# Performance work log

Measured on AMD Instinct MI355X. Metric: run time of the kernel, lower is better.

Reference implementation:

```python
import jax, jax.numpy as jnp
import numpy as np

N_NODES = 100000
N_EDGES = 1600000
D_IN, D_HID, D_OUT = 128, 64, 16


def _glorot(key, shape):
    lim = float(np.sqrt(6.0 / (shape[0] + shape[1])))
    return jax.random.uniform(key, shape, jnp.float32, -lim, lim)


def setup_inputs() -> dict:
    key = jax.random.key(0)
    k1, k2, k3 = jax.random.split(key, 3)
    x = jax.random.normal(k1, (N_NODES, D_IN), dtype=jnp.float32)
    edge_index = jax.random.randint(k2, (2, N_EDGES), 0, N_NODES, dtype=jnp.int64)
    kw1, kw2 = jax.random.split(k3)
    W1 = _glorot(kw1, (D_IN, D_HID))
    b1 = jnp.zeros((D_HID,), jnp.float32)
    W2 = _glorot(kw2, (D_HID, D_OUT))
    b2 = jnp.zeros((D_OUT,), jnp.float32)
    return {"x": x, "edge_index": edge_index, "W1": W1, "b1": b1, "W2": W2, "b2": b2}


def _gcn_conv(h, W, b, src, dst, norm, n_nodes):
    # PyG GCNConv: linear first, then normalized neighbor aggregation, then bias.
    h = h @ W                                        # [N, d_out]
    msg = h[src] * norm[:, None]                     # gather over edges(+self loops)
    out = jax.ops.segment_sum(msg, dst, num_segments=n_nodes)  # scatter-add
    return out + b


def reference(x, edge_index, W1, b1, W2, b2):
    n = x.shape[0]
    loop = jnp.arange(n, dtype=edge_index.dtype)
    src = jnp.concatenate([edge_index[0], loop])     # add self loops
    dst = jnp.concatenate([edge_index[1], loop])
    # symmetric normalization D^-1/2 (A+I) D^-1/2
    deg = jax.ops.segment_sum(jnp.ones(src.shape[0], x.dtype), dst, num_segments=n)
    dinv = jnp.where(deg > 0, jax.lax.rsqrt(jnp.maximum(deg, 1e-12)), 0.0)
    norm = dinv[src] * dinv[dst]                     # [E+N]

    out = _gcn_conv(x, W1, b1, src, dst, norm, n)
    out = jax.nn.sigmoid(out)
    # dropout p=0.5 with training=False -> identity (eval mode)
    out = _gcn_conv(out, W2, b2, src, dst, norm, n)
    return jax.nn.log_softmax(out, axis=1)
```

## Files before the change

kernel.cpp:

```cpp
#include <hip/hip_runtime.h>
#include <hip/hip_bf16.h>


constexpr int D_IN  = 128;
constexpr int D_HID = 64;
constexpr int D_OUT = 16;

constexpr int WSHIFT  = 9;
constexpr int MAXB    = 256;
constexpr int BCAP    = 12288;
constexpr int CSRCAP  = 16384;
constexpr int BIN_CAP = 48;
constexpr int CHUNK   = 4096;

typedef __attribute__((ext_vector_type(8))) short bf16x8;
typedef __attribute__((ext_vector_type(4))) float f32x4;

__device__ inline float bflo(unsigned u){ return __uint_as_float(u << 16); }
__device__ inline float bfhi(unsigned u){ return __uint_as_float(u & 0xffff0000u); }
__device__ inline unsigned f2bu(float f){
    __hip_bfloat16 h = __float2bfloat16(f);
    return (unsigned)*reinterpret_cast<unsigned short*>(&h);
}
__device__ inline float sigf(float x){ return 1.0f / (1.0f + __expf(-x)); }

__global__ __launch_bounds__(256) void k_bucketize(
    const int* __restrict__ ei, const unsigned* __restrict__ xraw,
    int* __restrict__ flags, unsigned* __restrict__ gcur,
    unsigned* __restrict__ gbuf, int ne, int B)
{
    __shared__ unsigned bcnt[MAXB];
    __shared__ unsigned bbase[MAXB];
    __shared__ unsigned bins[MAXB * BIN_CAP];
    __shared__ int s_i64;

    const int t = threadIdx.x, lane = t & 63, wv = t >> 6;
    const int e0 = blockIdx.x * CHUNK;

    if (t < MAXB) bcnt[t] = 0u;
    if (wv == 0){
        int w = ei[2 * lane + 1];
        unsigned long long m = __ballot(w == 0);
        if (lane == 0) s_i64 = (__popcll(m) > 48) ? 1 : 0;
        if (blockIdx.x == 0){
            unsigned u = xraw[lane];
            unsigned h0 = u & 0xffffu, h1 = u >> 16;
            unsigned ex0 = (h0 >> 7) & 0xffu, ex1 = (h1 >> 7) & 0xffu;
            bool bad0 = !((h0 & 0x7fffu) == 0 || (ex0 >= 97 && ex0 <= 157));
            bool bad1 = !((h1 & 0x7fffu) == 0 || (ex1 >= 97 && ex1 <= 157));
            unsigned long long m0 = __ballot(bad0);
            unsigned long long m1 = __ballot(bad1);
            if (lane == 0){
                int bad = __popcll(m0) + __popcll(m1);
                flags[0] = (bad > 8) ? 0 : 1;
                flags[1] = s_i64;
            }
        }
    }
    __syncthreads();
    const int i64 = s_i64;
    const bool vec = ((ne & 1) == 0);

    #pragma unroll
    for (int k = 0; k < CHUNK / 512; ++k){
        int e = e0 + k * 512 + 2 * t;
        int s0, d0, s1, d1;
        int cntE = 0;
        if (vec && e < ne){
            if (i64){
                int4 sp = *(const int4*)&ei[2 * e];
                int4 dp = *(const int4*)&ei[2 * (ne + e)];
                s0 = sp.x; s1 = sp.z; d0 = dp.x; d1 = dp.z;
            } else {
                int2 sp = *(const int2*)&ei[e];
                int2 dp = *(const int2*)&ei[ne + e];
                s0 = sp.x; s1 = sp.y; d0 = dp.x; d1 = dp.y;
            }
            cntE = 2;
        } else {
            if (e < ne){
                if (i64){ s0 = ei[2*e]; d0 = ei[2*(ne+e)]; }
                else    { s0 = ei[e];   d0 = ei[ne+e]; }
                cntE = 1;
                if (e + 1 < ne){
                    if (i64){ s1 = ei[2*(e+1)]; d1 = ei[2*(ne+e+1)]; }
                    else    { s1 = ei[e+1];     d1 = ei[ne+e+1]; }
                    cntE = 2;
                }
            }
        }
        #pragma unroll
        for (int j = 0; j < 2; ++j){
            if (j < cntE){
                int s = j ? s1 : s0, d = j ? d1 : d0;
                int b = d >> WSHIFT;
                unsigned v = ((unsigned)s << WSHIFT) | ((unsigned)d & ((1u << WSHIFT) - 1));
                unsigned p = atomicAdd(&bcnt[b], 1u);
                if (p < (unsigned)BIN_CAP){
                    bins[b * BIN_CAP + p] = v;
                } else {
                    unsigned g = atomicAdd(&gcur[b], 1u);
                    gbuf[(size_t)b * BCAP + g] = v;
                }
            }
        }
    }
    __syncthreads();

    if (t < B){
        unsigned c = min(bcnt[t], (unsigned)BIN_CAP);
        bbase[t] = atomicAdd(&gcur[t], c);
    }
    __syncthreads();

    for (int b = wv; b < B; b += 4){
        unsigned c = min(bcnt[b], (unsigned)BIN_CAP);
        for (unsigned o = lane; o < c; o += 64)
            gbuf[(size_t)b * BCAP + bbase[b] + o] = bins[b * BIN_CAP + o];
    }
}

__global__ __launch_bounds__(1024) void k_build(
    const unsigned* __restrict__ gbuf, const unsigned* __restrict__ gcnt,
    unsigned* __restrict__ off, unsigned* __restrict__ offend,
    float* __restrict__ dinv, int* __restrict__ csr, int n, int B)
{
    __shared__ unsigned hist[512];
    __shared__ unsigned offl[512];
    __shared__ unsigned wsums[8];

    const int t = threadIdx.x, lane = t & 63, wv = t >> 6;
    const int b = blockIdx.x;
    const int base = b << WSHIFT;
    const int nodes = min(512, n - base);
    const unsigned bb = (unsigned)b * CSRCAP;

    if (t < 512) hist[t] = 0u;
    __syncthreads();
    const unsigned cnt = gcnt[b];
    const unsigned* mybuf = gbuf + (size_t)b * BCAP;

    for (unsigned i = t; i < cnt; i += 1024)
        atomicAdd(&hist[mybuf[i] & ((1u << WSHIFT) - 1)], 1u);
    __syncthreads();

    unsigned v = 0, p = 0, x = 0;
    if (t < 512){
        v = hist[t];
        p = (v + 7u) & ~7u;
        x = p;
        #pragma unroll
        for (int o = 1; o < 64; o <<= 1){
            unsigned y = __shfl_up(x, o, 64);
            if (lane >= o) x += y;
        }
        if (lane == 63) wsums[wv] = x;
    }
    __syncthreads();
    if (t == 0){
        unsigned run = 0;
        #pragma unroll
        for (int w = 0; w < 8; ++w){ unsigned tv = wsums[w]; wsums[w] = run; run += tv; }
    }
    __syncthreads();
    if (t < 512) offl[t] = x - p + wsums[wv];
    __syncthreads();

    if (t < nodes){
        off[base + t]    = bb + offl[t];
        offend[base + t] = bb + offl[t] + p;
        dinv[base + t]   = rsqrtf(1.0f + (float)v);
    }
    __syncthreads();

    if (t < 512) hist[t] = offl[t];
    __syncthreads();

    for (unsigned i = t; i < cnt; i += 1024){
        unsigned rec = mybuf[i];
        unsigned pos = atomicAdd(&hist[rec & ((1u << WSHIFT) - 1)], 1u);
        csr[bb + pos] = (int)(rec >> WSHIFT);
    }
    __syncthreads();

    if (t < nodes){
        unsigned s = offl[t] + v, e2 = offl[t] + p;
        for (unsigned j = s; j < e2; ++j) csr[bb + j] = n;
    }
}

__global__ __launch_bounds__(256) void k_linear1(
    const unsigned* __restrict__ xraw, const unsigned* __restrict__ w1raw,
    const int* __restrict__ flags, const float* __restrict__ dinv,
    unsigned short* __restrict__ h1s, int n)
{
    const int lane = threadIdx.x & 63;
    const int wv   = threadIdx.x >> 6;
    const int m = lane & 15, q = lane >> 4;
    const int isBf16 = flags[0];

    if (blockIdx.x == 0 && threadIdx.x < 16)
        ((uint2*)(h1s + (size_t)n * D_HID))[threadIdx.x] = make_uint2(0u, 0u);

    bf16x8 bfr[4][4];
    if (isBf16){
        const unsigned short* w = (const unsigned short*)w1raw;
        #pragma unroll
        for (int kc = 0; kc < 4; ++kc)
            #pragma unroll
            for (int ct = 0; ct < 4; ++ct)
                #pragma unroll
                for (int j = 0; j < 8; ++j)
                    bfr[kc][ct][j] = (short)w[(kc*32 + q*8 + j) * D_HID + ct*16 + m];
    } else {
        const float* w = (const float*)w1raw;
        #pragma unroll
        for (int kc = 0; kc < 4; ++kc)
            #pragma unroll
            for (int ct = 0; ct < 4; ++ct)
                #pragma unroll
                for (int j = 0; j < 8; ++j)
                    bfr[kc][ct][j] = (short)f2bu(w[(kc*32 + q*8 + j) * D_HID + ct*16 + m]);
    }

    const int ntiles = (n + 15) >> 4;
    for (int tile = blockIdx.x * 4 + wv; tile < ntiles; tile += gridDim.x * 4){
        const int node0 = tile << 4;
        int arow = node0 + m; if (arow >= n) arow = n - 1;
        f32x4 ac0 = {0,0,0,0}, ac1 = {0,0,0,0}, ac2 = {0,0,0,0}, ac3 = {0,0,0,0};
        #pragma unroll
        for (int kc = 0; kc < 4; ++kc){
            bf16x8 a;
            if (isBf16){
                uint4 u = *(const uint4*)((const unsigned short*)xraw + (size_t)arow * D_IN + kc*32 + q*8);
                a = *reinterpret_cast<bf16x8*>(&u);
            } else {
                const float* xp = (const float*)xraw + (size_t)arow * D_IN + kc*32 + q*8;
                float4 f0 = *(const float4*)xp;
                float4 f1 = *(const float4*)(xp + 4);
                a[0]=(short)f2bu(f0.x); a[1]=(short)f2bu(f0.y); a[2]=(short)f2bu(f0.z); a[3]=(short)f2bu(f0.w);
                a[4]=(short)f2bu(f1.x); a[5]=(short)f2bu(f1.y); a[6]=(short)f2bu(f1.z); a[7]=(short)f2bu(f1.w);
            }
            ac0 = __builtin_amdgcn_mfma_f32_16x16x32_bf16(a, bfr[kc][0], ac0, 0, 0, 0);
            ac1 = __builtin_amdgcn_mfma_f32_16x16x32_bf16(a, bfr[kc][1], ac1, 0, 0, 0);
            ac2 = __builtin_amdgcn_mfma_f32_16x16x32_bf16(a, bfr[kc][2], ac2, 0, 0, 0);
            ac3 = __builtin_amdgcn_mfma_f32_16x16x32_bf16(a, bfr[kc][3], ac3, 0, 0, 0);
        }
        #pragma unroll
        for (int i = 0; i < 4; ++i){
            int nr = node0 + q*4 + i;
            if (nr < n){
                float di = dinv[nr];
                unsigned short* o = h1s + (size_t)nr * D_HID + m;
                o[0]  = (unsigned short)f2bu(ac0[i] * di);
                o[16] = (unsigned short)f2bu(ac1[i] * di);
                o[32] = (unsigned short)f2bu(ac2[i] * di);
                o[48] = (unsigned short)f2bu(ac3[i] * di);
            }
        }
    }
}

__global__ __launch_bounds__(256) void k_aggA(
    const unsigned* __restrict__ off, const unsigned* __restrict__ offend,
    const int* __restrict__ csr_src,
    const float* __restrict__ dinv, const unsigned short* __restrict__ h1s,
    const unsigned* __restrict__ b1raw, const unsigned* __restrict__ w2raw,
    const int* __restrict__ flags,
    unsigned short* __restrict__ h2s, int n)
{
    __shared__ unsigned short act_s[16][72];

    const int lane = threadIdx.x & 63;
    const int wv   = threadIdx.x >> 6;
    const int grp  = lane >> 4;
    const int f    = lane & 15;
    const int dl   = wv * 4 + grp;
    const int d    = blockIdx.x * 16 + dl;
    const int isBf16 = flags[0];

    bf16x8 w2f[2];
    if (wv == 0){
        const int m0 = lane & 15, q0 = lane >> 4;
        if (isBf16){
            const unsigned short* w = (const unsigned short*)w2raw;
            #pragma unroll
            for (int kc = 0; kc < 2; ++kc)
                #pragma unroll
                for (int j = 0; j < 8; ++j)
                    w2f[kc][j] = (short)w[(kc*32 + q0*8 + j) * D_OUT + m0];
        } else {
            const float* w = (const float*)w2raw;
            #pragma unroll
            for (int kc = 0; kc < 2; ++kc)
                #pragma unroll
                for (int j = 0; j < 8; ++j)
                    w2f[kc][j] = (short)f2bu(w[(kc*32 + q0*8 + j) * D_OUT + m0]);
        }
        if (blockIdx.x == 0 && lane < 4)
            ((uint2*)(h2s + (size_t)n * D_OUT))[lane] = make_uint2(0u, 0u);
    }

    if (d < n){
        const int beg = (int)off[d], end = (int)offend[d];
        float a0=0.f, a1=0.f, a2=0.f, a3=0.f;
        for (int i = beg; i < end; i += 8){
            uint4 cA = *(const uint4*)&csr_src[i];
            uint4 cB = *(const uint4*)&csr_src[i + 4];
            uint2 u0 = *(const uint2*)&h1s[(size_t)(unsigned)cA.x * D_HID + f * 4];
            uint2 u1 = *(const uint2*)&h1s[(size_t)(unsigned)cA.y * D_HID + f * 4];
            uint2 u2 = *(const uint2*)&h1s[(size_t)(unsigned)cA.z * D_HID + f * 4];
            uint2 u3 = *(const uint2*)&h1s[(size_t)(unsigned)cA.w * D_HID + f * 4];
            uint2 u4 = *(const uint2*)&h1s[(size_t)(unsigned)cB.x * D_HID + f * 4];
            uint2 u5 = *(const uint2*)&h1s[(size_t)(unsigned)cB.y * D_HID + f * 4];
            uint2 u6 = *(const uint2*)&h1s[(size_t)(unsigned)cB.z * D_HID + f * 4];
            uint2 u7 = *(const uint2*)&h1s[(size_t)(unsigned)cB.w * D_HID + f * 4];
            a0 += bflo(u0.x) + bflo(u1.x) + bflo(u2.x) + bflo(u3.x)
                + bflo(u4.x) + bflo(u5.x) + bflo(u6.x) + bflo(u7.x);
            a1 += bfhi(u0.x) + bfhi(u1.x) + bfhi(u2.x) + bfhi(u3.x)
                + bfhi(u4.x) + bfhi(u5.x) + bfhi(u6.x) + bfhi(u7.x);
            a2 += bflo(u0.y) + bflo(u1.y) + bflo(u2.y) + bflo(u3.y)
                + bflo(u4.y) + bflo(u5.y) + bflo(u6.y) + bflo(u7.y);
            a3 += bfhi(u0.y) + bfhi(u1.y) + bfhi(u2.y) + bfhi(u3.y)
                + bfhi(u4.y) + bfhi(u5.y) + bfhi(u6.y) + bfhi(u7.y);
        }
        uint2 su = *(const uint2*)&h1s[(size_t)d * D_HID + f * 4];
        a0 += bflo(su.x); a1 += bfhi(su.x);
        a2 += bflo(su.y); a3 += bfhi(su.y);
        const float dd = dinv[d];
        float b0, b1v, b2v, b3v;
        if (isBf16){
            uint2 bu = ((const uint2*)b1raw)[f];
            b0 = bflo(bu.x); b1v = bfhi(bu.x); b2v = bflo(bu.y); b3v = bfhi(bu.y);
        } else {
            float4 bb = ((const float4*)b1raw)[f];
            b0 = bb.x; b1v = bb.y; b2v = bb.z; b3v = bb.w;
        }
        act_s[dl][f*4+0] = (unsigned short)f2bu(sigf(fmaf(a0, dd, b0)));
        act_s[dl][f*4+1] = (unsigned short)f2bu(sigf(fmaf(a1, dd, b1v)));
        act_s[dl][f*4+2] = (unsigned short)f2bu(sigf(fmaf(a2, dd, b2v)));
        act_s[dl][f*4+3] = (unsigned short)f2bu(sigf(fmaf(a3, dd, b3v)));
    } else {
        #pragma unroll
        for (int j = 0; j < 4; ++j) act_s[dl][f*4+j] = 0;
    }
    __syncthreads();

    if (wv == 0){
        const int m0 = lane & 15, q0 = lane >> 4;
        f32x4 acc = {0,0,0,0};
        #pragma unroll
        for (int kc = 0; kc < 2; ++kc){
            bf16x8 a;
            #pragma unroll
            for (int j = 0; j < 8; ++j)
                a[j] = (short)act_s[m0][kc*32 + q0*8 + j];
            acc = __builtin_amdgcn_mfma_f32_16x16x32_bf16(a, w2f[kc], acc, 0, 0, 0);
        }
        #pragma unroll
        for (int i = 0; i < 4; ++i){
            int nr = blockIdx.x * 16 + q0*4 + i;
            if (nr < n)
                h2s[(size_t)nr * D_OUT + m0] = (unsigned short)f2bu(acc[i] * dinv[nr]);
        }
    }
}

__global__ __launch_bounds__(256) void k_aggB(
    const unsigned* __restrict__ off, const unsigned* __restrict__ offend,
    const int* __restrict__ csr_src,
    const float* __restrict__ dinv, const unsigned short* __restrict__ h2s,
    const unsigned* __restrict__ b2raw, const int* __restrict__ flags,
    void* __restrict__ out, int n)
{
    const int lane = threadIdx.x & 63;
    const int wv   = threadIdx.x >> 6;
    const int grp  = lane >> 2;
    const int f    = lane & 3;
    const int d    = (blockIdx.x * 4 + wv) * 16 + grp;
    const int isBf16 = flags[0];
    if (d >= n) return;

    const int beg = (int)off[d], end = (int)offend[d];
    float a0=0.f, a1=0.f, a2=0.f, a3=0.f;
    for (int i = beg; i < end; i += 8){
        uint4 cA = *(const uint4*)&csr_src[i];
        uint4 cB = *(const uint4*)&csr_src[i + 4];
        uint2 u0 = *(const uint2*)&h2s[(size_t)(unsigned)cA.x * D_OUT + f * 4];
        uint2 u1 = *(const uint2*)&h2s[(size_t)(unsigned)cA.y * D_OUT + f * 4];
        uint2 u2 = *(const uint2*)&h2s[(size_t)(unsigned)cA.z * D_OUT + f * 4];
        uint2 u3 = *(const uint2*)&h2s[(size_t)(unsigned)cA.w * D_OUT + f * 4];
        uint2 u4 = *(const uint2*)&h2s[(size_t)(unsigned)cB.x * D_OUT + f * 4];
        uint2 u5 = *(const uint2*)&h2s[(size_t)(unsigned)cB.y * D_OUT + f * 4];
        uint2 u6 = *(const uint2*)&h2s[(size_t)(unsigned)cB.z * D_OUT + f * 4];
        uint2 u7 = *(const uint2*)&h2s[(size_t)(unsigned)cB.w * D_OUT + f * 4];
        a0 += bflo(u0.x) + bflo(u1.x) + bflo(u2.x) + bflo(u3.x)
            + bflo(u4.x) + bflo(u5.x) + bflo(u6.x) + bflo(u7.x);
        a1 += bfhi(u0.x) + bfhi(u1.x) + bfhi(u2.x) + bfhi(u3.x)
            + bfhi(u4.x) + bfhi(u5.x) + bfhi(u6.x) + bfhi(u7.x);
        a2 += bflo(u0.y) + bflo(u1.y) + bflo(u2.y) + bflo(u3.y)
            + bflo(u4.y) + bflo(u5.y) + bflo(u6.y) + bflo(u7.y);
        a3 += bfhi(u0.y) + bfhi(u1.y) + bfhi(u2.y) + bfhi(u3.y)
            + bfhi(u4.y) + bfhi(u5.y) + bfhi(u6.y) + bfhi(u7.y);
    }
    uint2 su = *(const uint2*)&h2s[(size_t)d * D_OUT + f * 4];
    a0 += bflo(su.x); a1 += bfhi(su.x);
    a2 += bflo(su.y); a3 += bfhi(su.y);
    const float dd = dinv[d];
    float b0, b1v, b2v, b3v;
    if (isBf16){
        uint2 bu = ((const uint2*)b2raw)[f];
        b0 = bflo(bu.x); b1v = bfhi(bu.x); b2v = bflo(bu.y); b3v = bfhi(bu.y);
    } else {
        float4 bb = ((const float4*)b2raw)[f];
        b0 = bb.x; b1v = bb.y; b2v = bb.z; b3v = bb.w;
    }
    a0 = fmaf(a0, dd, b0); a1 = fmaf(a1, dd, b1v);
    a2 = fmaf(a2, dd, b2v); a3 = fmaf(a3, dd, b3v);
    float m = fmaxf(fmaxf(a0, a1), fmaxf(a2, a3));
    m = fmaxf(m, __shfl_xor(m, 1, 4));
    m = fmaxf(m, __shfl_xor(m, 2, 4));
    float s = __expf(a0 - m) + __expf(a1 - m) + __expf(a2 - m) + __expf(a3 - m);
    s += __shfl_xor(s, 1, 4);
    s += __shfl_xor(s, 2, 4);
    float ls = m + __logf(s);
    if (isBf16){
        uint2 pk;
        pk.x = f2bu(a0 - ls) | (f2bu(a1 - ls) << 16);
        pk.y = f2bu(a2 - ls) | (f2bu(a3 - ls) << 16);
        *(uint2*)((__hip_bfloat16*)out + (size_t)d * D_OUT + f * 4) = pk;
    } else {
        float4 o4 = make_float4(a0 - ls, a1 - ls, a2 - ls, a3 - ls);
        *(float4*)((float*)out + (size_t)d * D_OUT + f * 4) = o4;
    }
}

extern "C" void kernel_launch(void* const* d_in, const int* in_sizes, int n_in,
                              void* d_out, int out_size, void* d_ws, size_t ws_size,
                              hipStream_t stream)
{
    const unsigned* xraw  = (const unsigned*)d_in[0];
    const int*      ei    = (const int*)d_in[1];
    const unsigned* w1raw = (const unsigned*)d_in[2];
    const unsigned* b1raw = (const unsigned*)d_in[3];
    const unsigned* w2raw = (const unsigned*)d_in[4];
    const unsigned* b2raw = (const unsigned*)d_in[5];

    const int n  = in_sizes[0] / D_IN;
    const int ne = in_sizes[1] / 2;
    const int B  = (n + ((1 << WSHIFT) - 1)) >> WSHIFT;

    size_t nAl = ((size_t)n + 255) & ~(size_t)255;
    int*            flags  = (int*)d_ws;
    unsigned*       gcur   = (unsigned*)d_ws + 64;
    float*          dinv   = (float*)(gcur + 256);
    unsigned*       off    = (unsigned*)(dinv + nAl);
    unsigned*       offend = off + nAl;
    int*            csr    = (int*)(offend + nAl);
    unsigned*       gbuf   = (unsigned*)(csr + (size_t)MAXB * CSRCAP);
    unsigned short* h1s    = (unsigned short*)(gbuf + (size_t)MAXB * BCAP);
    unsigned short* h2s    = h1s + (size_t)(n + 16) * D_HID;

    const int nchunk  = (ne + CHUNK - 1) / CHUNK;
    const int ntiles1 = (n + 15) / 16;
    const int grid1   = (ntiles1 + 3) / 4;

    hipMemsetAsync(gcur, 0, MAXB * sizeof(unsigned), stream);
    k_bucketize <<<nchunk, 256, 0, stream>>>(ei, xraw, flags, gcur, gbuf, ne, B);
    k_build     <<<B, 1024, 0, stream>>>(gbuf, gcur, off, offend, dinv, csr, n, B);

    k_linear1   <<<grid1, 256, 0, stream>>>(xraw, w1raw, flags, dinv, h1s, n);
    k_aggA      <<<(n + 15) / 16, 256, 0, stream>>>(off, offend, csr, dinv, h1s, b1raw, w2raw, flags, h2s, n);
    k_aggB      <<<(n + 63) / 64, 256, 0, stream>>>(off, offend, csr, dinv, h2s, b2raw, flags, d_out, n);
}
```

Baseline: 194.6 us.

## Fuse all GCN stages into one persistent kernel with grid-wide barriers

Replaces the five separate launches (bucketize, CSR build, linear1, layer-1 aggregation, layer-2 aggregation) with one persistent kernel sized at three blocks per CU. Atomic-counter grid barriers separate the phases, and each phase loops over its work items with a grid stride. This removes launch gaps and tail effects between stages. In exchange, the CSR build now runs on 256-thread blocks instead of 1024, the shared bins and chunk sizes are halved to fit the higher occupancy, and correctness relies on all blocks being co-resident for the spin barriers.

```diff
diff --git a/kernel.cpp b/kernel.cpp
--- a/kernel.cpp
+++ b/kernel.cpp
@@ -10,8 +10,8 @@
 constexpr int MAXB    = 256;
 constexpr int BCAP    = 12288;
 constexpr int CSRCAP  = 16384;
-constexpr int BIN_CAP = 48;
-constexpr int CHUNK   = 4096;
+constexpr int BIN_CAP = 24;
+constexpr int CHUNK   = 2048;
 
 typedef __attribute__((ext_vector_type(8))) short bf16x8;
 typedef __attribute__((ext_vector_type(4))) float f32x4;
@@ -24,20 +24,35 @@
 }
 __device__ inline float sigf(float x){ return 1.0f / (1.0f + __expf(-x)); }
 
-__global__ __launch_bounds__(256) void k_bucketize(
-    const int* __restrict__ ei, const unsigned* __restrict__ xraw,
-    int* __restrict__ flags, unsigned* __restrict__ gcur,
-    unsigned* __restrict__ gbuf, int ne, int B)
+__device__ inline void gbar(unsigned* ctr){
+    __syncthreads();
+    if (threadIdx.x == 0){
+        __threadfence();
+        __hip_atomic_fetch_add(ctr, 1u, __ATOMIC_RELEASE, __HIP_MEMORY_SCOPE_AGENT);
+        while (__hip_atomic_load(ctr, __ATOMIC_RELAXED, __HIP_MEMORY_SCOPE_AGENT) < gridDim.x)
+            __builtin_amdgcn_s_sleep(16);
+        __threadfence();
+    }
+    __syncthreads();
+}
+
+__global__ __launch_bounds__(256, 4) void k_mega(
+    const unsigned* __restrict__ xraw, const int* __restrict__ ei,
+    const unsigned* __restrict__ w1raw, const unsigned* __restrict__ b1raw,
+    const unsigned* __restrict__ w2raw, const unsigned* __restrict__ b2raw,
+    int* __restrict__ flags, unsigned* __restrict__ bar,
+    unsigned* __restrict__ gcur, unsigned* __restrict__ gbuf,
+    unsigned* __restrict__ off, unsigned* __restrict__ offend,
+    float* __restrict__ dinv, int* __restrict__ csr,
+    unsigned short* __restrict__ h1s, unsigned short* __restrict__ h2s,
+    void* __restrict__ out, int n, int ne, int B, int nchunk)
 {
-    __shared__ unsigned bcnt[MAXB];
-    __shared__ unsigned bbase[MAXB];
-    __shared__ unsigned bins[MAXB * BIN_CAP];
+    __shared__ unsigned smem[512 + MAXB * BIN_CAP];
     __shared__ int s_i64;
 
     const int t = threadIdx.x, lane = t & 63, wv = t >> 6;
-    const int e0 = blockIdx.x * CHUNK;
-
-    if (t < MAXB) bcnt[t] = 0u;
+    const int G = (int)gridDim.x;
+
     if (wv == 0){
         int w = ei[2 * lane + 1];
         unsigned long long m = __ballot(w == 0);
@@ -61,377 +76,362 @@
     const int i64 = s_i64;
     const bool vec = ((ne & 1) == 0);
 
-    #pragma unroll
-    for (int k = 0; k < CHUNK / 512; ++k){
-        int e = e0 + k * 512 + 2 * t;
-        int s0, d0, s1, d1;
-        int cntE = 0;
-        if (vec && e < ne){
-            if (i64){
-                int4 sp = *(const int4*)&ei[2 * e];
-                int4 dp = *(const int4*)&ei[2 * (ne + e)];
-                s0 = sp.x; s1 = sp.z; d0 = dp.x; d1 = dp.z;
+    {
+        unsigned* bcnt  = smem;
+        unsigned* bbase = smem + 256;
+        unsigned* bins  = smem + 512;
+
+        for (int ch = (int)blockIdx.x; ch < nchunk; ch += G){
+            if (t < MAXB) bcnt[t] = 0u;
+            __syncthreads();
+            const int e0 = ch * CHUNK;
+            #pragma unroll
+            for (int k = 0; k < CHUNK / 512; ++k){
+                int e = e0 + k * 512 + 2 * t;
+                int s0, d0, s1, d1;
+                int cntE = 0;
+                if (vec && e < ne){
+                    if (i64){
+                        int4 sp = *(const int4*)&ei[2 * e];
+                        int4 dp = *(const int4*)&ei[2 * (ne + e)];
+                        s0 = sp.x; s1 = sp.z; d0 = dp.x; d1 = dp.z;
+                    } else {
+                        int2 sp = *(const int2*)&ei[e];
+                        int2 dp = *(const int2*)&ei[ne + e];
+                        s0 = sp.x; s1 = sp.y; d0 = dp.x; d1 = dp.y;
+                    }
+                    cntE = 2;
+                } else {
+                    if (e < ne){
+                        if (i64){ s0 = ei[2*e]; d0 = ei[2*(ne+e)]; }
+                        else    { s0 = ei[e];   d0 = ei[ne+e]; }
+                        cntE = 1;
+                        if (e + 1 < ne){
+                            if (i64){ s1 = ei[2*(e+1)]; d1 = ei[2*(ne+e+1)]; }
+                            else    { s1 = ei[e+1];     d1 = ei[ne+e+1]; }
+                            cntE = 2;
+                        }
+                    }
+                }
+                #pragma unroll
+                for (int j = 0; j < 2; ++j){
+                    if (j < cntE){
+                        int s = j ? s1 : s0, d = j ? d1 : d0;
+                        int b = d >> WSHIFT;
+                        unsigned v = ((unsigned)s << WSHIFT) | ((unsigned)d & ((1u << WSHIFT) - 1));
+                        unsigned p = atomicAdd(&bcnt[b], 1u);
+                        if (p < (unsigned)BIN_CAP){
+                            bins[b * BIN_CAP + p] = v;
+                        } else {
+                            unsigned g2 = atomicAdd(&gcur[b], 1u);
+                            gbuf[(size_t)b * BCAP + g2] = v;
+                        }
+                    }
+                }
+            }
+            __syncthreads();
+            if (t < B){
+                unsigned c = min(bcnt[t], (unsigned)BIN_CAP);
+                bbase[t] = atomicAdd(&gcur[t], c);
+            }
+            __syncthreads();
+            for (int b = wv; b < B; b += 4){
+                unsigned c = min(bcnt[b], (unsigned)BIN_CAP);
+                unsigned ba = bbase[b];
+                for (unsigned o = (unsigned)lane; o < c; o += 64)
+                    gbuf[(size_t)b * BCAP + ba + o] = bins[b * BIN_CAP + o];
+            }
+            __syncthreads();
+        }
+    }
+
+    gbar(&bar[0]);
+
+    {
+        unsigned* hist  = smem;
+        unsigned* wsums = smem + 512;
+        for (int b = (int)blockIdx.x; b < B; b += G){
+            const int base = b << WSHIFT;
+            const int nodes = min(512, n - base);
+            const unsigned bb = (unsigned)b * CSRCAP;
+            hist[t] = 0u; hist[t + 256] = 0u;
+            __syncthreads();
+            const unsigned cnt = gcur[b];
+            const unsigned* mybuf = gbuf + (size_t)b * BCAP;
+            for (unsigned i = t; i < cnt; i += 256)
+                atomicAdd(&hist[mybuf[i] & ((1u << WSHIFT) - 1)], 1u);
+            __syncthreads();
+            unsigned v0 = hist[2*t], v1 = hist[2*t+1];
+            unsigned p0 = (v0 + 7u) & ~7u, p1 = (v1 + 7u) & ~7u;
+            unsigned x = p0 + p1, xi = x;
+            #pragma unroll
+            for (int o = 1; o < 64; o <<= 1){
+                unsigned y = __shfl_up(xi, o, 64);
+                if (lane >= o) xi += y;
+            }
+            if (lane == 63) wsums[wv] = xi;
+            __syncthreads();
+            if (t == 0){
+                unsigned run = 0;
+                #pragma unroll
+                for (int w8 = 0; w8 < 4; ++w8){ unsigned tv = wsums[w8]; wsums[w8] = run; run += tv; }
+            }
+            __syncthreads();
+            const unsigned ex = xi - x + wsums[wv];
+            if (2*t < nodes){
+                off[base + 2*t]    = bb + ex;
+                offend[base + 2*t] = bb + ex + p0;
+                dinv[base + 2*t]   = rsqrtf(1.0f + (float)v0);
+            }
+            if (2*t+1 < nodes){
+                off[base + 2*t+1]    = bb + ex + p0;
+                offend[base + 2*t+1] = bb + ex + p0 + p1;
+                dinv[base + 2*t+1]   = rsqrtf(1.0f + (float)v1);
+            }
+            __syncthreads();
+            hist[2*t] = ex; hist[2*t+1] = ex + p0;
+            __syncthreads();
+            for (unsigned i = t; i < cnt; i += 256){
+                unsigned rec = mybuf[i];
+                unsigned pos = atomicAdd(&hist[rec & ((1u << WSHIFT) - 1)], 1u);
+                csr[bb + pos] = (int)(rec >> WSHIFT);
+            }
+            __syncthreads();
+            if (2*t < nodes){
+                for (unsigned j2 = ex + v0; j2 < ex + p0; ++j2) csr[bb + j2] = n;
+            }
+            if (2*t+1 < nodes){
+                unsigned o1 = ex + p0;
+                for (unsigned j2 = o1 + v1; j2 < o1 + p1; ++j2) csr[bb + j2] = n;
+            }
+            __syncthreads();
+        }
+    }
+
+    gbar(&bar[1]);
+
+    const int isBf16 = flags[0];
+    if (blockIdx.x == 0 && t < 16)
+        ((uint2*)(h1s + (size_t)n * D_HID))[t] = make_uint2(0u, 0u);
+    {
+        const int m = lane & 15, q = lane >> 4;
+        const int ntiles = (n + 15) >> 4;
+        for (int tile = (int)blockIdx.x * 4 + wv; tile < ntiles; tile += G * 4){
+            const int node0 = tile << 4;
+            int arow = node0 + m; if (arow >= n) arow = n - 1;
+            f32x4 ac0 = {0,0,0,0}, ac1 = {0,0,0,0}, ac2 = {0,0,0,0}, ac3 = {0,0,0,0};
+            #pragma unroll
+            for (int kc = 0; kc < 4; ++kc){
+                bf16x8 a;
+                if (isBf16){
+                    uint4 u = *(const uint4*)((const unsigned short*)xraw + (size_t)arow * D_IN + kc*32 + q*8);
+                    a = *reinterpret_cast<bf16x8*>(&u);
+                } else {
+                    const float* xp = (const float*)xraw + (size_t)arow * D_IN + kc*32 + q*8;
+                    float4 f0 = *(const float4*)xp;
+                    float4 f1 = *(const float4*)(xp + 4);
+                    a[0]=(short)f2bu(f0.x); a[1]=(short)f2bu(f0.y); a[2]=(short)f2bu(f0.z); a[3]=(short)f2bu(f0.w);
+                    a[4]=(short)f2bu(f1.x); a[5]=(short)f2bu(f1.y); a[6]=(short)f2bu(f1.z); a[7]=(short)f2bu(f1.w);
+                }
+                bf16x8 b0, b1, b2, b3;
+                if (isBf16){
+                    const unsigned short* w = (const unsigned short*)w1raw;
+                    #pragma unroll
+                    for (int j = 0; j < 8; ++j){
+                        int r = (kc*32 + q*8 + j) * D_HID + m;
+                        b0[j] = (short)w[r];      b1[j] = (short)w[r + 16];
+                        b2[j] = (short)w[r + 32]; b3[j] = (short)w[r + 48];
+                    }
+                } else {
+                    const float* w = (const float*)w1raw;
+                    #pragma unroll
+                    for (int j = 0; j < 8; ++j){
+                        int r = (kc*32 + q*8 + j) * D_HID + m;
+                        b0[j] = (short)f2bu(w[r]);      b1[j] = (short)f2bu(w[r + 16]);
+                        b2[j] = (short)f2bu(w[r + 32]); b3[j] = (short)f2bu(w[r + 48]);
+                    }
+                }
+                ac0 = __builtin_amdgcn_mfma_f32_16x16x32_bf16(a, b0, ac0, 0, 0, 0);
+                ac1 = __builtin_amdgcn_mfma_f32_16x16x32_bf16(a, b1, ac1, 0, 0, 0);
+                ac2 = __builtin_amdgcn_mfma_f32_16x16x32_bf16(a, b2, ac2, 0, 0, 0);
+                ac3 = __builtin_amdgcn_mfma_f32_16x16x32_bf16(a, b3, ac3, 0, 0, 0);
+            }
+            #pragma unroll
+            for (int i = 0; i < 4; ++i){
+                int nr = node0 + q*4 + i;
+                if (nr < n){
+                    float di = dinv[nr];
+                    unsigned short* o = h1s + (size_t)nr * D_HID + m;
+                    o[0]  = (unsigned short)f2bu(ac0[i] * di);
+                    o[16] = (unsigned short)f2bu(ac1[i] * di);
+                    o[32] = (unsigned short)f2bu(ac2[i] * di);
+                    o[48] = (unsigned short)f2bu(ac3[i] * di);
+                }
+            }
+        }
+    }
+
+    gbar(&bar[2]);
+
+    {
+        unsigned short* act_s = (unsigned short*)smem;
+        const int grp = lane >> 4;
+        const int f   = lane & 15;
+        const int dl  = wv * 4 + grp;
+        const int m0 = lane & 15, q0 = lane >> 4;
+
+        bf16x8 w2f[2];
+        if (wv == 0){
+            if (isBf16){
+                const unsigned short* w = (const unsigned short*)w2raw;
+                #pragma unroll
+                for (int kc = 0; kc < 2; ++kc)
+                    #pragma unroll
+                    for (int j = 0; j < 8; ++j)
+                        w2f[kc][j] = (short)w[(kc*32 + q0*8 + j) * D_OUT + m0];
             } else {
-                int2 sp = *(const int2*)&ei[e];
-                int2 dp = *(const int2*)&ei[ne + e];
-                s0 = sp.x; s1 = sp.y; d0 = dp.x; d1 = dp.y;
-            }
-            cntE = 2;
-        } else {
-            if (e < ne){
-                if (i64){ s0 = ei[2*e]; d0 = ei[2*(ne+e)]; }
-                else    { s0 = ei[e];   d0 = ei[ne+e]; }
-                cntE = 1;
-                if (e + 1 < ne){
-                    if (i64){ s1 = ei[2*(e+1)]; d1 = ei[2*(ne+e+1)]; }
-                    else    { s1 = ei[e+1];     d1 = ei[ne+e+1]; }
-                    cntE = 2;
-                }
-            }
-        }
-        #pragma unroll
-        for (int j = 0; j < 2; ++j){
-            if (j < cntE){
-                int s = j ? s1 : s0, d = j ? d1 : d0;
-                int b = d >> WSHIFT;
-                unsigned v = ((unsigned)s << WSHIFT) | ((unsigned)d & ((1u << WSHIFT) - 1));
-                unsigned p = atomicAdd(&bcnt[b], 1u);
-                if (p < (unsigned)BIN_CAP){
-                    bins[b * BIN_CAP + p] = v;
+                const float* w = (const float*)w2raw;
+                #pragma unroll
+                for (int kc = 0; kc < 2; ++kc)
+                    #pragma unroll
+                    for (int j = 0; j < 8; ++j)
+                        w2f[kc][j] = (short)f2bu(w[(kc*32 + q0*8 + j) * D_OUT + m0]);
+            }
+            if (blockIdx.x == 0 && lane < 4)
+                ((uint2*)(h2s + (size_t)n * D_OUT))[lane] = make_uint2(0u, 0u);
+        }
+
+        const int ng = (n + 15) >> 4;
+        for (int g = (int)blockIdx.x; g < ng; g += G){
+            const int d = g * 16 + dl;
+            if (d < n){
+                const int beg = (int)off[d], end = (int)offend[d];
+                float a0=0.f, a1=0.f, a2=0.f, a3=0.f;
+                for (int i = beg; i < end; i += 8){
+                    uint4 cA = *(const uint4*)&csr[i];
+                    uint4 cB = *(const uint4*)&csr[i + 4];
+                    uint2 u0 = *(const uint2*)&h1s[(size_t)(unsigned)cA.x * D_HID + f * 4];
+                    uint2 u1 = *(const uint2*)&h1s[(size_t)(unsigned)cA.y * D_HID + f * 4];
+                    uint2 u2 = *(const uint2*)&h1s[(size_t)(unsigned)cA.z * D_HID + f * 4];
+                    uint2 u3 = *(const uint2*)&h1s[(size_t)(unsigned)cA.w * D_HID + f * 4];
+                    uint2 u4 = *(const uint2*)&h1s[(size_t)(unsigned)cB.x * D_HID + f * 4];
+                    uint2 u5 = *(const uint2*)&h1s[(size_t)(unsigned)cB.y * D_HID + f * 4];
+                    uint2 u6 = *(const uint2*)&h1s[(size_t)(unsigned)cB.z * D_HID + f * 4];
+                    uint2 u7 = *(const uint2*)&h1s[(size_t)(unsigned)cB.w * D_HID + f * 4];
+                    a0 += bflo(u0.x) + bflo(u1.x) + bflo(u2.x) + bflo(u3.x)
+                        + bflo(u4.x) + bflo(u5.x) + bflo(u6.x) + bflo(u7.x);
+                    a1 += bfhi(u0.x) + bfhi(u1.x) + bfhi(u2.x) + bfhi(u3.x)
+                        + bfhi(u4.x) + bfhi(u5.x) + bfhi(u6.x) + bfhi(u7.x);
+                    a2 += bflo(u0.y) + bflo(u1.y) + bflo(u2.y) + bflo(u3.y)
+                        + bflo(u4.y) + bflo(u5.y) + bflo(u6.y) + bflo(u7.y);
+                    a3 += bfhi(u0.y) + bfhi(u1.y) + bfhi(u2.y) + bfhi(u3.y)
+                        + bfhi(u4.y) + bfhi(u5.y) + bfhi(u6.y) + bfhi(u7.y);
+                }
+                uint2 su = *(const uint2*)&h1s[(size_t)d * D_HID + f * 4];
+                a0 += bflo(su.x); a1 += bfhi(su.x);
+                a2 += bflo(su.y); a3 += bfhi(su.y);
+                const float dd = dinv[d];
+                float b0, b1v, b2v, b3v;
+                if (isBf16){
+                    uint2 bu = ((const uint2*)b1raw)[f];
+                    b0 = bflo(bu.x); b1v = bfhi(bu.x); b2v = bflo(bu.y); b3v = bfhi(bu.y);
                 } else {
-                    unsigned g = atomicAdd(&gcur[b], 1u);
-                    gbuf[(size_t)b * BCAP + g] = v;
-                }
-            }
-        }
-    }
-    __syncthreads();
-
-    if (t < B){
-        unsigned c = min(bcnt[t], (unsigned)BIN_CAP);
-        bbase[t] = atomicAdd(&gcur[t], c);
-    }
-    __syncthreads();
-
-    for (int b = wv; b < B; b += 4){
-        unsigned c = min(bcnt[b], (unsigned)BIN_CAP);
-        for (unsigned o = lane; o < c; o += 64)
-            gbuf[(size_t)b * BCAP + bbase[b] + o] = bins[b * BIN_CAP + o];
-    }
-}
-
-__global__ __launch_bounds__(1024) void k_build(
-    const unsigned* __restrict__ gbuf, const unsigned* __restrict__ gcnt,
-    unsigned* __restrict__ off, unsigned* __restrict__ offend,
-    float* __restrict__ dinv, int* __restrict__ csr, int n, int B)
-{
-    __shared__ unsigned hist[512];
-    __shared__ unsigned offl[512];
-    __shared__ unsigned wsums[8];
-
-    const int t = threadIdx.x, lane = t & 63, wv = t >> 6;
-    const int b = blockIdx.x;
-    const int base = b << WSHIFT;
-    const int nodes = min(512, n - base);
-    const unsigned bb = (unsigned)b * CSRCAP;
-
-    if (t < 512) hist[t] = 0u;
-    __syncthreads();
-    const unsigned cnt = gcnt[b];
-    const unsigned* mybuf = gbuf + (size_t)b * BCAP;
-
-    for (unsigned i = t; i < cnt; i += 1024)
-        atomicAdd(&hist[mybuf[i] & ((1u << WSHIFT) - 1)], 1u);
-    __syncthreads();
-
-    unsigned v = 0, p = 0, x = 0;
-    if (t < 512){
-        v = hist[t];
-        p = (v + 7u) & ~7u;
-        x = p;
-        #pragma unroll
-        for (int o = 1; o < 64; o <<= 1){
-            unsigned y = __shfl_up(x, o, 64);
-            if (lane >= o) x += y;
-        }
-        if (lane == 63) wsums[wv] = x;
-    }
-    __syncthreads();
-    if (t == 0){
-        unsigned run = 0;
-        #pragma unroll
-        for (int w = 0; w < 8; ++w){ unsigned tv = wsums[w]; wsums[w] = run; run += tv; }
-    }
-    __syncthreads();
-    if (t < 512) offl[t] = x - p + wsums[wv];
-    __syncthreads();
-
-    if (t < nodes){
-        off[base + t]    = bb + offl[t];
-        offend[base + t] = bb + offl[t] + p;
-        dinv[base + t]   = rsqrtf(1.0f + (float)v);
-    }
-    __syncthreads();
-
-    if (t < 512) hist[t] = offl[t];
-    __syncthreads();
-
-    for (unsigned i = t; i < cnt; i += 1024){
-        unsigned rec = mybuf[i];
-        unsigned pos = atomicAdd(&hist[rec & ((1u << WSHIFT) - 1)], 1u);
-        csr[bb + pos] = (int)(rec >> WSHIFT);
-    }
-    __syncthreads();
-
-    if (t < nodes){
-        unsigned s = offl[t] + v, e2 = offl[t] + p;
-        for (unsigned j = s; j < e2; ++j) csr[bb + j] = n;
-    }
-}
-
-__global__ __launch_bounds__(256) void k_linear1(
-    const unsigned* __restrict__ xraw, const unsigned* __restrict__ w1raw,
-    const int* __restrict__ flags, const float* __restrict__ dinv,
-    unsigned short* __restrict__ h1s, int n)
-{
-    const int lane = threadIdx.x & 63;
-    const int wv   = threadIdx.x >> 6;
-    const int m = lane & 15, q = lane >> 4;
-    const int isBf16 = flags[0];
-
-    if (blockIdx.x == 0 && threadIdx.x < 16)
-        ((uint2*)(h1s + (size_t)n * D_HID))[threadIdx.x] = make_uint2(0u, 0u);
-
-    bf16x8 bfr[4][4];
-    if (isBf16){
-        const unsigned short* w = (const unsigned short*)w1raw;
-        #pragma unroll
-        for (int kc = 0; kc < 4; ++kc)
-            #pragma unroll
-            for (int ct = 0; ct < 4; ++ct)
-                #pragma unroll
-                for (int j = 0; j < 8; ++j)
-                    bfr[kc][ct][j] = (short)w[(kc*32 + q*8 + j) * D_HID + ct*16 + m];
-    } else {
-        const float* w = (const float*)w1raw;
-        #pragma unroll
-        for (int kc = 0; kc < 4; ++kc)
-            #pragma unroll
-            for (int ct = 0; ct < 4; ++ct)
-                #pragma unroll
-                for (int j = 0; j < 8; ++j)
-                    bfr[kc][ct][j] = (short)f2bu(w[(kc*32 + q*8 + j) * D_HID + ct*16 + m]);
-    }
-
-    const int ntiles = (n + 15) >> 4;
-    for (int tile = blockIdx.x * 4 + wv; tile < ntiles; tile += gridDim.x * 4){
-        const int node0 = tile << 4;
-        int arow = node0 + m; if (arow >= n) arow = n - 1;
-        f32x4 ac0 = {0,0,0,0}, ac1 = {0,0,0,0}, ac2 = {0,0,0,0}, ac3 = {0,0,0,0};
-        #pragma unroll
-        for (int kc = 0; kc < 4; ++kc){
-            bf16x8 a;
+                    float4 bb4 = ((const float4*)b1raw)[f];
+                    b0 = bb4.x; b1v = bb4.y; b2v = bb4.z; b3v = bb4.w;
+                }
+                act_s[dl*72 + f*4 + 0] = (unsigned short)f2bu(sigf(fmaf(a0, dd, b0)));
+                act_s[dl*72 + f*4 + 1] = (unsigned short)f2bu(sigf(fmaf(a1, dd, b1v)));
+                act_s[dl*72 + f*4 + 2] = (unsigned short)f2bu(sigf(fmaf(a2, dd, b2v)));
+                act_s[dl*72 + f*4 + 3] = (unsigned short)f2bu(sigf(fmaf(a3, dd, b3v)));
+            } else {
+                #pragma unroll
+                for (int j = 0; j < 4; ++j) act_s[dl*72 + f*4 + j] = 0;
+            }
+            __syncthreads();
+
+            if (wv == 0){
+                f32x4 acc = {0,0,0,0};
+                #pragma unroll
+                for (int kc = 0; kc < 2; ++kc){
+                    bf16x8 a;
+                    #pragma unroll
+                    for (int j = 0; j < 8; ++j)
+                        a[j] = (short)act_s[m0*72 + kc*32 + q0*8 + j];
+                    acc = __builtin_amdgcn_mfma_f32_16x16x32_bf16(a, w2f[kc], acc, 0, 0, 0);
+                }
+                #pragma unroll
+                for (int i = 0; i < 4; ++i){
+                    int nr = g * 16 + q0*4 + i;
+                    if (nr < n)
+                        h2s[(size_t)nr * D_OUT + m0] = (unsigned short)f2bu(acc[i] * dinv[nr]);
+                }
+            }
+            __syncthreads();
+        }
+    }
+
+    gbar(&bar[3]);
+
+    {
+        const int grp = lane >> 2;
+        const int f   = lane & 3;
+        const int nw = (n + 15) >> 4;
+        for (int w = (int)blockIdx.x * 4 + wv; w < nw; w += G * 4){
+            const int d = w * 16 + grp;
+            if (d >= n) continue;
+            const int beg = (int)off[d], end = (int)offend[d];
+            float a0=0.f, a1=0.f, a2=0.f, a3=0.f;
+            for (int i = beg; i < end; i += 8){
+                uint4 cA = *(const uint4*)&csr[i];
+                uint4 cB = *(const uint4*)&csr[i + 4];
+                uint2 u0 = *(const uint2*)&h2s[(size_t)(unsigned)cA.x * D_OUT + f * 4];
+                uint2 u1 = *(const uint2*)&h2s[(size_t)(unsigned)cA.y * D_OUT + f * 4];
+                uint2 u2 = *(const uint2*)&h2s[(size_t)(unsigned)cA.z * D_OUT + f * 4];
+                uint2 u3 = *(const uint2*)&h2s[(size_t)(unsigned)cA.w * D_OUT + f * 4];
+                uint2 u4 = *(const uint2*)&h2s[(size_t)(unsigned)cB.x * D_OUT + f * 4];
+                uint2 u5 = *(const uint2*)&h2s[(size_t)(unsigned)cB.y * D_OUT + f * 4];
+                uint2 u6 = *(const uint2*)&h2s[(size_t)(unsigned)cB.z * D_OUT + f * 4];
+                uint2 u7 = *(const uint2*)&h2s[(size_t)(unsigned)cB.w * D_OUT + f * 4];
+                a0 += bflo(u0.x) + bflo(u1.x) + bflo(u2.x) + bflo(u3.x)
+                    + bflo(u4.x) + bflo(u5.x) + bflo(u6.x) + bflo(u7.x);
+                a1 += bfhi(u0.x) + bfhi(u1.x) + bfhi(u2.x) + bfhi(u3.x)
+                    + bfhi(u4.x) + bfhi(u5.x) + bfhi(u6.x) + bfhi(u7.x);
+                a2 += bflo(u0.y) + bflo(u1.y) + bflo(u2.y) + bflo(u3.y)
+                    + bflo(u4.y) + bflo(u5.y) + bflo(u6.y) + bflo(u7.y);
+                a3 += bfhi(u0.y) + bfhi(u1.y) + bfhi(u2.y) + bfhi(u3.y)
+                    + bfhi(u4.y) + bfhi(u5.y) + bfhi(u6.y) + bfhi(u7.y);
+            }
+            uint2 su = *(const uint2*)&h2s[(size_t)d * D_OUT + f * 4];
+            a0 += bflo(su.x); a1 += bfhi(su.x);
+            a2 += bflo(su.y); a3 += bfhi(su.y);
+            const float dd = dinv[d];
+            float b0, b1v, b2v, b3v;
             if (isBf16){
-                uint4 u = *(const uint4*)((const unsigned short*)xraw + (size_t)arow * D_IN + kc*32 + q*8);
-                a = *reinterpret_cast<bf16x8*>(&u);
+                uint2 bu = ((const uint2*)b2raw)[f];
+                b0 = bflo(bu.x); b1v = bfhi(bu.x); b2v = bflo(bu.y); b3v = bfhi(bu.y);
             } else {
-                const float* xp = (const float*)xraw + (size_t)arow * D_IN + kc*32 + q*8;
-                float4 f0 = *(const float4*)xp;
-                float4 f1 = *(const float4*)(xp + 4);
-                a[0]=(short)f2bu(f0.x); a[1]=(short)f2bu(f0.y); a[2]=(short)f2bu(f0.z); a[3]=(short)f2bu(f0.w);
-                a[4]=(short)f2bu(f1.x); a[5]=(short)f2bu(f1.y); a[6]=(short)f2bu(f1.z); a[7]=(short)f2bu(f1.w);
-            }
-            ac0 = __builtin_amdgcn_mfma_f32_16x16x32_bf16(a, bfr[kc][0], ac0, 0, 0, 0);
-            ac1 = __builtin_amdgcn_mfma_f32_16x16x32_bf16(a, bfr[kc][1], ac1, 0, 0, 0);
-            ac2 = __builtin_amdgcn_mfma_f32_16x16x32_bf16(a, bfr[kc][2], ac2, 0, 0, 0);
-            ac3 = __builtin_amdgcn_mfma_f32_16x16x32_bf16(a, bfr[kc][3], ac3, 0, 0, 0);
-        }
-        #pragma unroll
-        for (int i = 0; i < 4; ++i){
-            int nr = node0 + q*4 + i;
-            if (nr < n){
-                float di = dinv[nr];
-                unsigned short* o = h1s + (size_t)nr * D_HID + m;
-                o[0]  = (unsigned short)f2bu(ac0[i] * di);
-                o[16] = (unsigned short)f2bu(ac1[i] * di);
-                o[32] = (unsigned short)f2bu(ac2[i] * di);
-                o[48] = (unsigned short)f2bu(ac3[i] * di);
-            }
-        }
-    }
-}
-
-__global__ __launch_bounds__(256) void k_aggA(
-    const unsigned* __restrict__ off, const unsigned* __restrict__ offend,
-    const int* __restrict__ csr_src,
-    const float* __restrict__ dinv, const unsigned short* __restrict__ h1s,
-    const unsigned* __restrict__ b1raw, const unsigned* __restrict__ w2raw,
-    const int* __restrict__ flags,
-    unsigned short* __restrict__ h2s, int n)
-{
-    __shared__ unsigned short act_s[16][72];
-
-    const int lane = threadIdx.x & 63;
-    const int wv   = threadIdx.x >> 6;
-    const int grp  = lane >> 4;
-    const int f    = lane & 15;
-    const int dl   = wv * 4 + grp;
-    const int d    = blockIdx.x * 16 + dl;
-    const int isBf16 = flags[0];
-
-    bf16x8 w2f[2];
-    if (wv == 0){
-        const int m0 = lane & 15, q0 = lane >> 4;
-        if (isBf16){
-            const unsigned short* w = (const unsigned short*)w2raw;
-            #pragma unroll
-            for (int kc = 0; kc < 2; ++kc)
-                #pragma unroll
-                for (int j = 0; j < 8; ++j)
-                    w2f[kc][j] = (short)w[(kc*32 + q0*8 + j) * D_OUT + m0];
-        } else {
-            const float* w = (const float*)w2raw;
-            #pragma unroll
-            for (int kc = 0; kc < 2; ++kc)
-                #pragma unroll
-                for (int j = 0; j < 8; ++j)
-                    w2f[kc][j] = (short)f2bu(w[(kc*32 + q0*8 + j) * D_OUT + m0]);
-        }
-        if (blockIdx.x == 0 && lane < 4)
-            ((uint2*)(h2s + (size_t)n * D_OUT))[lane] = make_uint2(0u, 0u);
-    }
-
-    if (d < n){
-        const int beg = (int)off[d], end = (int)offend[d];
-        float a0=0.f, a1=0.f, a2=0.f, a3=0.f;
-        for (int i = beg; i < end; i += 8){
-            uint4 cA = *(const uint4*)&csr_src[i];
-            uint4 cB = *(const uint4*)&csr_src[i + 4];
-            uint2 u0 = *(const uint2*)&h1s[(size_t)(unsigned)cA.x * D_HID + f * 4];
-            uint2 u1 = *(const uint2*)&h1s[(size_t)(unsigned)cA.y * D_HID + f * 4];
-            uint2 u2 = *(const uint2*)&h1s[(size_t)(unsigned)cA.z * D_HID + f * 4];
-            uint2 u3 = *(const uint2*)&h1s[(size_t)(unsigned)cA.w * D_HID + f * 4];
-            uint2 u4 = *(const uint2*)&h1s[(size_t)(unsigned)cB.x * D_HID + f * 4];
-            uint2 u5 = *(const uint2*)&h1s[(size_t)(unsigned)cB.y * D_HID + f * 4];
-            uint2 u6 = *(const uint2*)&h1s[(size_t)(unsigned)cB.z * D_HID + f * 4];
-            uint2 u7 = *(const uint2*)&h1s[(size_t)(unsigned)cB.w * D_HID + f * 4];
-            a0 += bflo(u0.x) + bflo(u1.x) + bflo(u2.x) + bflo(u3.x)
-                + bflo(u4.x) + bflo(u5.x) + bflo(u6.x) + bflo(u7.x);
-            a1 += bfhi(u0.x) + bfhi(u1.x) + bfhi(u2.x) + bfhi(u3.x)
-                + bfhi(u4.x) + bfhi(u5.x) + bfhi(u6.x) + bfhi(u7.x);
-            a2 += bflo(u0.y) + bflo(u1.y) + bflo(u2.y) + bflo(u3.y)
-                + bflo(u4.y) + bflo(u5.y) + bflo(u6.y) + bflo(u7.y);
-            a3 += bfhi(u0.y) + bfhi(u1.y) + bfhi(u2.y) + bfhi(u3.y)
-                + bfhi(u4.y) + bfhi(u5.y) + bfhi(u6.y) + bfhi(u7.y);
-        }
-        uint2 su = *(const uint2*)&h1s[(size_t)d * D_HID + f * 4];
-        a0 += bflo(su.x); a1 += bfhi(su.x);
-        a2 += bflo(su.y); a3 += bfhi(su.y);
-        const float dd = dinv[d];
-        float b0, b1v, b2v, b3v;
-        if (isBf16){
-            uint2 bu = ((const uint2*)b1raw)[f];
-            b0 = bflo(bu.x); b1v = bfhi(bu.x); b2v = bflo(bu.y); b3v = bfhi(bu.y);
-        } else {
-            float4 bb = ((const float4*)b1raw)[f];
-            b0 = bb.x; b1v = bb.y; b2v = bb.z; b3v = bb.w;
-        }
-        act_s[dl][f*4+0] = (unsigned short)f2bu(sigf(fmaf(a0, dd, b0)));
-        act_s[dl][f*4+1] = (unsigned short)f2bu(sigf(fmaf(a1, dd, b1v)));
-        act_s[dl][f*4+2] = (unsigned short)f2bu(sigf(fmaf(a2, dd, b2v)));
-        act_s[dl][f*4+3] = (unsigned short)f2bu(sigf(fmaf(a3, dd, b3v)));
-    } else {
-        #pragma unroll
-        for (int j = 0; j < 4; ++j) act_s[dl][f*4+j] = 0;
-    }
-    __syncthreads();
-
-    if (wv == 0){
-        const int m0 = lane & 15, q0 = lane >> 4;
-        f32x4 acc = {0,0,0,0};
-        #pragma unroll
-        for (int kc = 0; kc < 2; ++kc){
-            bf16x8 a;
-            #pragma unroll
-            for (int j = 0; j < 8; ++j)
-                a[j] = (short)act_s[m0][kc*32 + q0*8 + j];
-            acc = __builtin_amdgcn_mfma_f32_16x16x32_bf16(a, w2f[kc], acc, 0, 0, 0);
-        }
-        #pragma unroll
-        for (int i = 0; i < 4; ++i){
-            int nr = blockIdx.x * 16 + q0*4 + i;
-            if (nr < n)
-                h2s[(size_t)nr * D_OUT + m0] = (unsigned short)f2bu(acc[i] * dinv[nr]);
-        }
-    }
-}
-
-__global__ __launch_bounds__(256) void k_aggB(
-    const unsigned* __restrict__ off, const unsigned* __restrict__ offend,
-    const int* __restrict__ csr_src,
-    const float* __restrict__ dinv, const unsigned short* __restrict__ h2s,
-    const unsigned* __restrict__ b2raw, const int* __restrict__ flags,
-    void* __restrict__ out, int n)
-{
-    const int lane = threadIdx.x & 63;
-    const int wv   = threadIdx.x >> 6;
-    const int grp  = lane >> 2;
-    const int f    = lane & 3;
-    const int d    = (blockIdx.x * 4 + wv) * 16 + grp;
-    const int isBf16 = flags[0];
-    if (d >= n) return;
-
-    const int beg = (int)off[d], end = (int)offend[d];
-    float a0=0.f, a1=0.f, a2=0.f, a3=0.f;
-    for (int i = beg; i < end; i += 8){
-        uint4 cA = *(const uint4*)&csr_src[i];
-        uint4 cB = *(const uint4*)&csr_src[i + 4];
-        uint2 u0 = *(const uint2*)&h2s[(size_t)(unsigned)cA.x * D_OUT + f * 4];
-        uint2 u1 = *(const uint2*)&h2s[(size_t)(unsigned)cA.y * D_OUT + f * 4];
-        uint2 u2 = *(const uint2*)&h2s[(size_t)(unsigned)cA.z * D_OUT + f * 4];
-        uint2 u3 = *(const uint2*)&h2s[(size_t)(unsigned)cA.w * D_OUT + f * 4];
-        uint2 u4 = *(const uint2*)&h2s[(size_t)(unsigned)cB.x * D_OUT + f * 4];
-        uint2 u5 = *(const uint2*)&h2s[(size_t)(unsigned)cB.y * D_OUT + f * 4];
-        uint2 u6 = *(const uint2*)&h2s[(size_t)(unsigned)cB.z * D_OUT + f * 4];
-        uint2 u7 = *(const uint2*)&h2s[(size_t)(unsigned)cB.w * D_OUT + f * 4];
-        a0 += bflo(u0.x) + bflo(u1.x) + bflo(u2.x) + bflo(u3.x)
-            + bflo(u4.x) + bflo(u5.x) + bflo(u6.x) + bflo(u7.x);
-        a1 += bfhi(u0.x) + bfhi(u1.x) + bfhi(u2.x) + bfhi(u3.x)
-            + bfhi(u4.x) + bfhi(u5.x) + bfhi(u6.x) + bfhi(u7.x);
-        a2 += bflo(u0.y) + bflo(u1.y) + bflo(u2.y) + bflo(u3.y)
-            + bflo(u4.y) + bflo(u5.y) + bflo(u6.y) + bflo(u7.y);
-        a3 += bfhi(u0.y) + bfhi(u1.y) + bfhi(u2.y) + bfhi(u3.y)
-            + bfhi(u4.y) + bfhi(u5.y) + bfhi(u6.y) + bfhi(u7.y);
-    }
-    uint2 su = *(const uint2*)&h2s[(size_t)d * D_OUT + f * 4];
-    a0 += bflo(su.x); a1 += bfhi(su.x);
-    a2 += bflo(su.y); a3 += bfhi(su.y);
-    const float dd = dinv[d];
-    float b0, b1v, b2v, b3v;
-    if (isBf16){
-        uint2 bu = ((const uint2*)b2raw)[f];
-        b0 = bflo(bu.x); b1v = bfhi(bu.x); b2v = bflo(bu.y); b3v = bfhi(bu.y);
-    } else {
-        float4 bb = ((const float4*)b2raw)[f];
-        b0 = bb.x; b1v = bb.y; b2v = bb.z; b3v = bb.w;
-    }
-    a0 = fmaf(a0, dd, b0); a1 = fmaf(a1, dd, b1v);
-    a2 = fmaf(a2, dd, b2v); a3 = fmaf(a3, dd, b3v);
-    float m = fmaxf(fmaxf(a0, a1), fmaxf(a2, a3));
-    m = fmaxf(m, __shfl_xor(m, 1, 4));
-    m = fmaxf(m, __shfl_xor(m, 2, 4));
-    float s = __expf(a0 - m) + __expf(a1 - m) + __expf(a2 - m) + __expf(a3 - m);
-    s += __shfl_xor(s, 1, 4);
-    s += __shfl_xor(s, 2, 4);
-    float ls = m + __logf(s);
-    if (isBf16){
-        uint2 pk;
-        pk.x = f2bu(a0 - ls) | (f2bu(a1 - ls) << 16);
-        pk.y = f2bu(a2 - ls) | (f2bu(a3 - ls) << 16);
-        *(uint2*)((__hip_bfloat16*)out + (size_t)d * D_OUT + f * 4) = pk;
-    } else {
-        float4 o4 = make_float4(a0 - ls, a1 - ls, a2 - ls, a3 - ls);
-        *(float4*)((float*)out + (size_t)d * D_OUT + f * 4) = o4;
+                float4 bb4 = ((const float4*)b2raw)[f];
+                b0 = bb4.x; b1v = bb4.y; b2v = bb4.z; b3v = bb4.w;
+            }
+            a0 = fmaf(a0, dd, b0); a1 = fmaf(a1, dd, b1v);
+            a2 = fmaf(a2, dd, b2v); a3 = fmaf(a3, dd, b3v);
+            float m = fmaxf(fmaxf(a0, a1), fmaxf(a2, a3));
+            m = fmaxf(m, __shfl_xor(m, 1, 4));
+            m = fmaxf(m, __shfl_xor(m, 2, 4));
+            float s = __expf(a0 - m) + __expf(a1 - m) + __expf(a2 - m) + __expf(a3 - m);
+            s += __shfl_xor(s, 1, 4);
+            s += __shfl_xor(s, 2, 4);
+            float ls = m + __logf(s);
+            if (isBf16){
+                uint2 pk;
+                pk.x = f2bu(a0 - ls) | (f2bu(a1 - ls) << 16);
+                pk.y = f2bu(a2 - ls) | (f2bu(a3 - ls) << 16);
+                *(uint2*)((__hip_bfloat16*)out + (size_t)d * D_OUT + f * 4) = pk;
+            } else {
+                float4 o4 = make_float4(a0 - ls, a1 - ls, a2 - ls, a3 - ls);
+                *(float4*)((float*)out + (size_t)d * D_OUT + f * 4) = o4;
+            }
+        }
     }
 }
 
@@ -452,24 +452,31 @@
 
     size_t nAl = ((size_t)n + 255) & ~(size_t)255;
     int*            flags  = (int*)d_ws;
+    unsigned*       bar    = (unsigned*)d_ws + 32;
     unsigned*       gcur   = (unsigned*)d_ws + 64;
-    float*          dinv   = (float*)(gcur + 256);
-    unsigned*       off    = (unsigned*)(dinv + nAl);
+    float*          dinvp  = (float*)(gcur + 256);
+    unsigned*       off    = (unsigned*)(dinvp + nAl);
     unsigned*       offend = off + nAl;
     int*            csr    = (int*)(offend + nAl);
     unsigned*       gbuf   = (unsigned*)(csr + (size_t)MAXB * CSRCAP);
     unsigned short* h1s    = (unsigned short*)(gbuf + (size_t)MAXB * BCAP);
     unsigned short* h2s    = h1s + (size_t)(n + 16) * D_HID;
 
-    const int nchunk  = (ne + CHUNK - 1) / CHUNK;
-    const int ntiles1 = (n + 15) / 16;
-    const int grid1   = (ntiles1 + 3) / 4;
-
-    hipMemsetAsync(gcur, 0, MAXB * sizeof(unsigned), stream);
-    k_bucketize <<<nchunk, 256, 0, stream>>>(ei, xraw, flags, gcur, gbuf, ne, B);
-    k_build     <<<B, 1024, 0, stream>>>(gbuf, gcur, off, offend, dinv, csr, n, B);
-
-    k_linear1   <<<grid1, 256, 0, stream>>>(xraw, w1raw, flags, dinv, h1s, n);
-    k_aggA      <<<(n + 15) / 16, 256, 0, stream>>>(off, offend, csr, dinv, h1s, b1raw, w2raw, flags, h2s, n);
-    k_aggB      <<<(n + 63) / 64, 256, 0, stream>>>(off, offend, csr, dinv, h2s, b2raw, flags, d_out, n);
+    const int nchunk = (ne + CHUNK - 1) / CHUNK;
+
+    static int s_cus = 0;
+    if (s_cus == 0){
+        int dev = 0, c = 0;
+        (void)hipGetDevice(&dev);
+        if (hipDeviceGetAttribute(&c, hipDeviceAttributeMultiprocessorCount, dev) != hipSuccess || c <= 0)
+            c = 256;
+        s_cus = c;
+    }
+    const int G = s_cus * 3;
+
+    hipMemsetAsync((char*)d_ws + 32 * sizeof(unsigned), 0, (32 + 256) * sizeof(unsigned), stream);
+
+    k_mega<<<G, 256, 0, stream>>>(xraw, ei, w1raw, b1raw, w2raw, b2raw,
+                                  flags, bar, gcur, gbuf, off, offend, dinvp,
+                                  csr, h1s, h2s, d_out, n, ne, B, nchunk);
 }
```

Result: slower. 774.6 us (+298.0%).
